# Kernel tuning notes

Measured on AMD Instinct MI355X. Metric: run time of the kernel, lower is better.

The kernel has to match this reference:

```python
import jax, jax.numpy as jnp
import numpy as np

B = 524288   # particles
H = 128      # hidden_size
E = 64       # embed_dim
NT = 512     # num trajectories
IN = 16 + 9 + E  # fc1 input dim = 89
EPS = 1e-6


def setup_inputs() -> dict:
    key = jax.random.key(0)
    ks = jax.random.split(key, 12)
    w = lambda k, shp, fan_in: (jax.random.normal(k, shp, dtype=jnp.float32)
                                / np.sqrt(fan_in).astype(np.float32))
    return {
        "F": jax.random.normal(ks[0], (B, 3, 3), dtype=jnp.float32),
        "C": jax.random.normal(ks[1], (B, 3, 3), dtype=jnp.float32),
        "traj_id": 7,
        "latent": jax.random.normal(ks[2], (NT, E), dtype=jnp.float32),
        "W1": w(ks[3], (IN, H), IN), "b1": jnp.zeros((H,), jnp.float32),
        "W2": w(ks[4], (H, H), H),   "b2": jnp.zeros((H,), jnp.float32),
        "W3": w(ks[5], (H, H), H),   "b3": jnp.zeros((H,), jnp.float32),
        "W4": w(ks[6], (H, H), H),   "b4": jnp.zeros((H,), jnp.float32),
        "W5": w(ks[7], (H, H), H),   "b5": jnp.zeros((H,), jnp.float32),
        "W6": w(ks[8], (H, H), H),   "b6": jnp.zeros((H,), jnp.float32),
        "W7": w(ks[9], (H, 9), H),   "b7": jnp.zeros((9,), jnp.float32),
    }


def _strain_features(F):
    # FFt: [B,3,3]; J = clamp(det F); J1 = clamp(F00); sigma: 3 singular values
    FFt = jnp.einsum('bij,bkj->bik', F, F)
    J = jnp.maximum(jnp.linalg.det(F), EPS)
    J1 = jnp.maximum(F[:, 0, 0], EPS)
    sigma = jnp.linalg.svd(F, compute_uv=False)  # descending, like torch.svd
    return jnp.concatenate([
        FFt.reshape(-1, 9),
        jnp.log(J)[:, None], sigma, J[:, None],
        jnp.log(J1)[:, None], J1[:, None],
    ], axis=-1)  # [B,16]


def reference(F, C, traj_id, latent,
              W1, b1, W2, b2, W3, b3, W4, b4, W5, b5, W6, b6, W7, b7):
    strain = _strain_features(F)                                   # [B,16]
    lat = jnp.broadcast_to(latent[traj_id], (F.shape[0], latent.shape[1]))
    x = jnp.concatenate([strain, C.reshape(-1, 9), lat], axis=-1)  # [B,89]
    g = lambda z: jax.nn.gelu(z, approximate=False)  # exact, matches torch GELU
    x = g(x @ W1 + b1)
    x = g(x @ W2 + b2)
    x = g(x @ W3 + b3)
    x = g(x @ W4 + b4)
    x = g(x @ W5 + b5)
    x = g(x @ W6 + b6)
    out = (x @ W7 + b7).reshape(-1, 3, 3)
    return 0.5 * (out + jnp.swapaxes(out, 1, 2))  # symmetric stress [B,3,3]
```

## Files before the change

### kernel.cpp

```cpp
#include <hip/hip_runtime.h>
#include <hip/hip_bf16.h>
#include <math.h>

#define BPART   524288
#define NBLK    (BPART / 128)
#define W7_OFF  98304
#define WB_N    102400
#define BIAS_N  800
#define PREP_N  (WB_N + BIAS_N)

typedef __bf16 bf16x8 __attribute__((ext_vector_type(8)));
typedef float  f32x16 __attribute__((ext_vector_type(16)));
typedef float  f32x4  __attribute__((ext_vector_type(4)));
typedef float  f32x2  __attribute__((ext_vector_type(2)));

#define MFMA __builtin_amdgcn_mfma_f32_32x32x16_bf16

__device__ __forceinline__ unsigned short f2bf(float f) {
  union { float f; unsigned u; } v; v.f = f;
  unsigned r = v.u + 0x7fffu + ((v.u >> 16) & 1u);
  return (unsigned short)(r >> 16);
}
__device__ __forceinline__ unsigned pack_bf16(float a, float b) {
  unsigned ua = __builtin_bit_cast(unsigned, a) + 0x8000u;
  unsigned ub = __builtin_bit_cast(unsigned, b) + 0x8000u;
  return __builtin_amdgcn_perm(ub, ua, 0x07060302u);
}
__device__ __forceinline__ int swz(int row, int col) {
  return (row << 7) | ((((col >> 3) ^ (row & 7)) << 3) | (col & 7));
}

__device__ __forceinline__ f32x2 pk_mul(f32x2 a, f32x2 b) {
  f32x2 d; asm("v_pk_mul_f32 %0, %1, %2" : "=v"(d) : "v"(a), "v"(b)); return d;
}
__device__ __forceinline__ f32x2 pk_fma(f32x2 a, f32x2 b, f32x2 c) {
  f32x2 d; asm("v_pk_fma_f32 %0, %1, %2, %3" : "=v"(d) : "v"(a), "v"(b), "v"(c)); return d;
}
__device__ __forceinline__ f32x2 gelu2(f32x2 z) {
  const f32x2 c1 = {0.1029432f, 0.1029432f};
  const f32x2 c0 = {2.30220818f, 2.30220818f};
  f32x2 z2 = pk_mul(z, z);
  f32x2 t  = pk_fma(z2, c1, c0);
  f32x2 yp = pk_mul(z, t);
  float e0 = __builtin_amdgcn_exp2f(-yp.x);
  float e1 = __builtin_amdgcn_exp2f(-yp.y);
  float r0 = __builtin_amdgcn_rcpf(e0 + 1.0f);
  float r1 = __builtin_amdgcn_rcpf(e1 + 1.0f);
  f32x2 g; g.x = z.x * r0; g.y = z.y * r1;
  return g;
}
__device__ __forceinline__ void cp16(const void* g, void* l) {
  __builtin_amdgcn_global_load_lds(
      (const __attribute__((address_space(1))) void*)g,
      (__attribute__((address_space(3))) void*)l, 16, 0, 0);
}

__global__ void prep_weights(
    const float* __restrict__ W1, const float* __restrict__ W2,
    const float* __restrict__ W3, const float* __restrict__ W4,
    const float* __restrict__ W5, const float* __restrict__ W6,
    const float* __restrict__ W7,
    const float* __restrict__ b1, const float* __restrict__ b2,
    const float* __restrict__ b3, const float* __restrict__ b4,
    const float* __restrict__ b5, const float* __restrict__ b6,
    const float* __restrict__ b7,
    unsigned short* __restrict__ wsb, float* __restrict__ wsf)
{
  int idx = blockIdx.x * 256 + threadIdx.x;
  if (idx < WB_N) {
    unsigned short v = 0;
    if (idx < W7_OFF) {
      int l = idx >> 14;
      int o = idx & 16383;
      int n = o >> 7, e = o & 127;
      int k = (((e >> 3) ^ (n & 7)) << 3) | (e & 7);
      const float* W = (l==0)?W1:(l==1)?W2:(l==2)?W3:(l==3)?W4:(l==4)?W5:W6;
      float x = (l == 0) ? ((k < 89) ? W[k*128 + n] : 0.0f)
                         : W[k*128 + n];
      v = f2bf(x);
    } else {
      int o = idx - W7_OFF;
      int n = o >> 7, e = o & 127;
      int k = (((e >> 3) ^ (n & 7)) << 3) | (e & 7);
      v = (n < 9) ? f2bf(W7[k*9 + n]) : (unsigned short)0;
    }
    wsb[idx] = v;
  } else if (idx < PREP_N) {
    int r = idx - WB_N;
    float x;
    if (r < 768) {
      int l = r >> 7, n = r & 127;
      const float* bb = (l==0)?b1:(l==1)?b2:(l==2)?b3:(l==3)?b4:(l==4)?b5:b6;
      x = bb[n];
    } else {
      int n = r - 768;
      x = (n < 9) ? b7[n] : 0.0f;
    }
    wsf[r] = x;
  }
}

__global__ __launch_bounds__(256, 2) void stress_mlp(
    const float* __restrict__ F, const float* __restrict__ Cmat,
    const int* __restrict__ traj, const float* __restrict__ latent,
    const unsigned short* __restrict__ wst, const float* __restrict__ wsf,
    float* __restrict__ out)
{
  __shared__ __align__(16) unsigned short act_s[128 * 128];
  __shared__ __align__(16) unsigned short wt_s[128 * 128];

  const int tid  = threadIdx.x;
  const int lane = tid & 63;
  const int wid  = tid >> 6;
  const int lm   = lane & 31;
  const int lk   = lane >> 5;
  const int m0   = (wid >> 1) << 6;
  const int n0   = (wid & 1) << 6;
  const int pbase = (int)blockIdx.x << 7;

  {
    const char* src = (const char*)wst;
    char* dst = (char*)wt_s;
    #pragma unroll
    for (int i = 0; i < 8; ++i)
      cp16(src + i*4096 + tid*16, dst + i*4096 + tid*16);
  }

  if (tid < 128) {
    const int row = tid;
    const int p   = pbase + row;
    float f[9];
    #pragma unroll
    for (int i = 0; i < 9; ++i) f[i] = F[p * 9 + i];
    float fft[9];
    #pragma unroll
    for (int i = 0; i < 3; ++i)
      #pragma unroll
      for (int k = 0; k < 3; ++k)
        fft[i*3+k] = f[i*3]*f[k*3] + f[i*3+1]*f[k*3+1] + f[i*3+2]*f[k*3+2];
    float det = f[0]*(f[4]*f[8]-f[5]*f[7]) - f[1]*(f[3]*f[8]-f[5]*f[6])
              + f[2]*(f[3]*f[7]-f[4]*f[6]);
    float J  = fmaxf(det, 1e-6f);
    float J1 = fmaxf(f[0], 1e-6f);
    float a00=fft[0], a01=fft[1], a02=fft[2], a11=fft[4], a12=fft[5], a22=fft[8];
    float q  = (a00+a11+a22) * (1.0f/3.0f);
    float d0 = a00-q, d1 = a11-q, d2 = a22-q;
    float p2 = d0*d0 + d1*d1 + d2*d2 + 2.0f*(a01*a01 + a02*a02 + a12*a12);
    float e0, e1, e2;
    if (p2 < 1e-14f) { e0 = e1 = e2 = q; }
    else {
      float pp  = sqrtf(p2 * (1.0f/6.0f));
      float inv = 1.0f / pp;
      float b00=d0*inv, b11=d1*inv, b22=d2*inv, b01=a01*inv, b02=a02*inv, b12=a12*inv;
      float detb = b00*(b11*b22-b12*b12) - b01*(b01*b22-b12*b02) + b02*(b01*b12-b11*b02);
      float rr = 0.5f * detb;
      rr = fminf(fmaxf(rr, -1.0f), 1.0f);
      float pr = acosf(rr) * (1.0f / (3.0f * 6.2831853071795864f));
      e0 = q + 2.0f*pp*__builtin_amdgcn_cosf(pr);
      e2 = q + 2.0f*pp*__builtin_amdgcn_cosf(pr + (1.0f/3.0f));
      e1 = 3.0f*q - e0 - e2;
    }
    float s0 = sqrtf(fmaxf(e0, 0.f));
    float s1 = sqrtf(fmaxf(e1, 0.f));
    float s2 = sqrtf(fmaxf(e2, 0.f));
    #pragma unroll
    for (int i = 0; i < 9; ++i) act_s[swz(row, i)] = f2bf(fft[i]);
    act_s[swz(row,  9)] = f2bf(logf(J));
    act_s[swz(row, 10)] = f2bf(s0);
    act_s[swz(row, 11)] = f2bf(s1);
    act_s[swz(row, 12)] = f2bf(s2);
    act_s[swz(row, 13)] = f2bf(J);
    act_s[swz(row, 14)] = f2bf(logf(J1));
    act_s[swz(row, 15)] = f2bf(J1);
    #pragma unroll
    for (int i = 0; i < 9; ++i) act_s[swz(row, 16 + i)] = f2bf(Cmat[p*9 + i]);
  } else {
    const int row = tid - 128;
    const int t = traj[0];
    const float* lat = latent + t * 64;
    for (int j = 0; j < 64; ++j) act_s[swz(row, 25 + j)] = f2bf(lat[j]);
    for (int j = 89; j < 128; ++j) act_s[swz(row, j)] = 0;
  }

  const int mr0 = m0 + lm,      mr1 = m0 + 32 + lm;
  const int nr0 = n0 + lm,      nr1 = n0 + 32 + lm;

  f32x16 acc[2][2];
  union BF { f32x16 v; f32x4 q[4]; };

  for (int l = 0; l < 6; ++l) {
    BF bias[2];
    const float* bl = wsf + (l << 7);
    #pragma unroll
    for (int tn = 0; tn < 2; ++tn)
      #pragma unroll
      for (int qq = 0; qq < 4; ++qq)
        bias[tn].q[qq] = *(const f32x4*)(bl + n0 + (tn << 5) + (qq << 3) + (lk << 2));

    __syncthreads();

    {
      bf16x8 x0 = *(const bf16x8*)&act_s[(mr0 << 7) + ((lk ^ (mr0 & 7)) << 3)];
      bf16x8 x1 = *(const bf16x8*)&act_s[(mr1 << 7) + ((lk ^ (mr1 & 7)) << 3)];
      bf16x8 w0 = *(const bf16x8*)&wt_s[(nr0 << 7) + ((lk ^ (nr0 & 7)) << 3)];
      bf16x8 w1 = *(const bf16x8*)&wt_s[(nr1 << 7) + ((lk ^ (nr1 & 7)) << 3)];
      acc[0][0] = MFMA(w0, x0, bias[0].v, 0, 0, 0);
      acc[0][1] = MFMA(w0, x1, bias[0].v, 0, 0, 0);
      acc[1][0] = MFMA(w1, x0, bias[1].v, 0, 0, 0);
      acc[1][1] = MFMA(w1, x1, bias[1].v, 0, 0, 0);
    }
    #pragma unroll
    for (int kk = 1; kk < 8; ++kk) {
      const int kc = (kk << 1) + lk;
      bf16x8 x0 = *(const bf16x8*)&act_s[(mr0 << 7) + ((kc ^ (mr0 & 7)) << 3)];
      bf16x8 x1 = *(const bf16x8*)&act_s[(mr1 << 7) + ((kc ^ (mr1 & 7)) << 3)];
      bf16x8 w0 = *(const bf16x8*)&wt_s[(nr0 << 7) + ((kc ^ (nr0 & 7)) << 3)];
      bf16x8 w1 = *(const bf16x8*)&wt_s[(nr1 << 7) + ((kc ^ (nr1 & 7)) << 3)];
      acc[0][0] = MFMA(w0, x0, acc[0][0], 0, 0, 0);
      acc[0][1] = MFMA(w0, x1, acc[0][1], 0, 0, 0);
      acc[1][0] = MFMA(w1, x0, acc[1][0], 0, 0, 0);
      acc[1][1] = MFMA(w1, x1, acc[1][1], 0, 0, 0);
    }
    __syncthreads();

    if (l < 5) {
      const char* src = (const char*)(wst + ((l + 1) << 14));
      char* dst = (char*)wt_s;
      #pragma unroll
      for (int i = 0; i < 8; ++i)
        cp16(src + i*4096 + tid*16, dst + i*4096 + tid*16);
    } else {
      const char* src = (const char*)(wst + W7_OFF);
      char* dst = (char*)wt_s;
      #pragma unroll
      for (int i = 0; i < 2; ++i)
        cp16(src + i*4096 + tid*16, dst + i*4096 + tid*16);
    }

    #pragma unroll
    for (int tm = 0; tm < 2; ++tm) {
      const int m    = m0 + (tm << 5) + lm;
      const int rowb = m << 7;
      const int rx   = m & 7;
      #pragma unroll
      for (int tn = 0; tn < 2; ++tn) {
        const int cb = ((n0 + (tn << 5)) >> 3);
        #pragma unroll
        for (int q = 0; q < 4; ++q) {
          f32x2 za; za.x = acc[tn][tm][4*q + 0]; za.y = acc[tn][tm][4*q + 1];
          f32x2 zb; zb.x = acc[tn][tm][4*q + 2]; zb.y = acc[tn][tm][4*q + 3];
          f32x2 ga = gelu2(za);
          f32x2 gb = gelu2(zb);
          uint2 u;
          u.x = pack_bf16(ga.x, ga.y);
          u.y = pack_bf16(gb.x, gb.y);
          const int off = rowb + (((cb + q) ^ rx) << 3) + (lk << 2);
          *reinterpret_cast<uint2*>(&act_s[off]) = u;
        }
      }
    }
  }

  {
    BF bias7;
    #pragma unroll
    for (int qq = 0; qq < 4; ++qq)
      bias7.q[qq] = *(const f32x4*)(wsf + 768 + (qq << 3) + (lk << 2));

    __syncthreads();

    f32x16 acc7[2];
    if ((wid & 1) == 0) {
      {
        bf16x8 x0 = *(const bf16x8*)&act_s[(mr0 << 7) + ((lk ^ (mr0 & 7)) << 3)];
        bf16x8 x1 = *(const bf16x8*)&act_s[(mr1 << 7) + ((lk ^ (mr1 & 7)) << 3)];
        bf16x8 w0 = *(const bf16x8*)&wt_s[(lm << 7) + ((lk ^ (lm & 7)) << 3)];
        acc7[0] = MFMA(w0, x0, bias7.v, 0, 0, 0);
        acc7[1] = MFMA(w0, x1, bias7.v, 0, 0, 0);
      }
      #pragma unroll
      for (int kk = 1; kk < 8; ++kk) {
        const int kc = (kk << 1) + lk;
        bf16x8 x0 = *(const bf16x8*)&act_s[(mr0 << 7) + ((kc ^ (mr0 & 7)) << 3)];
        bf16x8 x1 = *(const bf16x8*)&act_s[(mr1 << 7) + ((kc ^ (mr1 & 7)) << 3)];
        bf16x8 w0 = *(const bf16x8*)&wt_s[(lm << 7) + ((kc ^ (lm & 7)) << 3)];
        acc7[0] = MFMA(w0, x0, acc7[0], 0, 0, 0);
        acc7[1] = MFMA(w0, x1, acc7[1], 0, 0, 0);
      }
    }
    __syncthreads();

    float* ots = (float*)wt_s;
    if ((wid & 1) == 0) {
      #pragma unroll
      for (int tm = 0; tm < 2; ++tm) {
        const int m = m0 + (tm << 5) + lm;
        #pragma unroll
        for (int j = 0; j < 4; ++j)
          ots[m * 9 + (lk << 2) + j] = acc7[tm][j];
        if (lk == 0) ots[m * 9 + 8] = acc7[tm][4];
      }
    }
    __syncthreads();

    if (tid < 128) {
      const int row = tid;
      float z[9];
      #pragma unroll
      for (int i = 0; i < 9; ++i) z[i] = ots[row * 9 + i];
      #pragma unroll
      for (int rr = 0; rr < 3; ++rr)
        #pragma unroll
        for (int cc = 0; cc < 3; ++cc)
          ots[row * 9 + rr*3 + cc] = 0.5f * (z[rr*3+cc] + z[cc*3+rr]);
    }
    __syncthreads();

    float4* dst = (float4*)(out + (size_t)pbase * 9);
    const float4* srcv = (const float4*)ots;
    for (int s = tid; s < 288; s += 256) dst[s] = srcv[s];
  }
}

extern "C" void kernel_launch(void* const* d_in, const int* in_sizes, int n_in,
                              void* d_out, int out_size, void* d_ws, size_t ws_size,
                              hipStream_t stream) {
  const float* F   = (const float*)d_in[0];
  const float* C   = (const float*)d_in[1];
  const int*   trj = (const int*)d_in[2];
  const float* lat = (const float*)d_in[3];
  const float* W1  = (const float*)d_in[4];
  const float* b1  = (const float*)d_in[5];
  const float* W2  = (const float*)d_in[6];
  const float* b2  = (const float*)d_in[7];
  const float* W3  = (const float*)d_in[8];
  const float* b3  = (const float*)d_in[9];
  const float* W4  = (const float*)d_in[10];
  const float* b4  = (const float*)d_in[11];
  const float* W5  = (const float*)d_in[12];
  const float* b5  = (const float*)d_in[13];
  const float* W6  = (const float*)d_in[14];
  const float* b6  = (const float*)d_in[15];
  const float* W7  = (const float*)d_in[16];
  const float* b7  = (const float*)d_in[17];

  unsigned short* wsb = (unsigned short*)d_ws;
  float* wsf = (float*)((char*)d_ws + WB_N * 2);

  prep_weights<<<dim3((PREP_N + 255) / 256), dim3(256), 0, stream>>>(
      W1, W2, W3, W4, W5, W6, W7, b1, b2, b3, b4, b5, b6, b7, wsb, wsf);
  stress_mlp<<<dim3(NBLK), dim3(256), 0, stream>>>(
      F, C, trj, lat, wsb, wsf, (float*)d_out);
}
```

Baseline: 287.6 us.

## Keep activations in registers across layers via permuted weight output ordering

Weight columns and biases are permuted at prep time so that each MFMA accumulator layout maps directly onto the next layer's B-operand register layout. Activations now stay in registers between layers instead of being written to and re-read from a shared-memory activation tile. That removes the act_s buffer, halves LDS use and allows the launch bound of 4 blocks per CU, with each wave owning 32 particles across all 128 outputs. Risks include higher register pressure from 32 packed activation registers plus four accumulators, and a permutation mapping that must be exactly right for correctness.

```diff
diff --git a/kernel.cpp b/kernel.cpp
--- a/kernel.cpp
+++ b/kernel.cpp
@@ -15,6 +15,9 @@
 typedef float  f32x2  __attribute__((ext_vector_type(2)));
 
 #define MFMA __builtin_amdgcn_mfma_f32_32x32x16_bf16
+#define UNROLL _Pragma("unroll")
+
+union XU { unsigned u[4]; bf16x8 v; };
 
 __device__ __forceinline__ unsigned short f2bf(float f) {
   union { float f; unsigned u; } v; v.f = f;
@@ -26,8 +29,10 @@
   unsigned ub = __builtin_bit_cast(unsigned, b) + 0x8000u;
   return __builtin_amdgcn_perm(ub, ua, 0x07060302u);
 }
-__device__ __forceinline__ int swz(int row, int col) {
-  return (row << 7) | ((((col >> 3) ^ (row & 7)) << 3) | (col & 7));
+
+__device__ __forceinline__ int sigma(int n) {
+  int c = ((n >> 5) << 2) | ((n >> 3) & 3);
+  return ((c >> 1) << 4) | (((n >> 2) & 1) << 3) | ((c & 1) << 2) | (n & 3);
 }
 
 __device__ __forceinline__ f32x2 pk_mul(f32x2 a, f32x2 b) {
@@ -74,15 +79,17 @@
       int o = idx & 16383;
       int n = o >> 7, e = o & 127;
       int k = (((e >> 3) ^ (n & 7)) << 3) | (e & 7);
+      int sn = sigma(n);
       const float* W = (l==0)?W1:(l==1)?W2:(l==2)?W3:(l==3)?W4:(l==4)?W5:W6;
-      float x = (l == 0) ? ((k < 89) ? W[k*128 + n] : 0.0f)
-                         : W[k*128 + n];
+      float x = (l == 0) ? ((k < 89) ? W[k*128 + sn] : 0.0f)
+                         : W[k*128 + sn];
       v = f2bf(x);
     } else {
       int o = idx - W7_OFF;
       int n = o >> 7, e = o & 127;
       int k = (((e >> 3) ^ (n & 7)) << 3) | (e & 7);
-      v = (n < 9) ? f2bf(W7[k*9 + n]) : (unsigned short)0;
+      int sn = sigma(n);
+      v = (sn < 9) ? f2bf(W7[k*9 + sn]) : (unsigned short)0;
     }
     wsb[idx] = v;
   } else if (idx < PREP_N) {
@@ -91,235 +98,241 @@
     if (r < 768) {
       int l = r >> 7, n = r & 127;
       const float* bb = (l==0)?b1:(l==1)?b2:(l==2)?b3:(l==3)?b4:(l==4)?b5:b6;
-      x = bb[n];
+      x = bb[sigma(n)];
     } else {
       int n = r - 768;
-      x = (n < 9) ? b7[n] : 0.0f;
+      int sn = sigma(n);
+      x = (sn < 9) ? b7[sn] : 0.0f;
     }
     wsf[r] = x;
   }
 }
 
-__global__ __launch_bounds__(256, 2) void stress_mlp(
+#define MFMA_LAYER(NKK)                                                       \
+  {                                                                           \
+    const float* bls_ = (const float*)((const char*)wt_s + 32768);            \
+    UNROLL                                                                    \
+    for (int kk = 0; kk < (NKK); ++kk) {                                      \
+      XU x_;                                                                  \
+      x_.u[0] = xw[4*kk+0]; x_.u[1] = xw[4*kk+1];                             \
+      x_.u[2] = xw[4*kk+2]; x_.u[3] = xw[4*kk+3];                             \
+      const int ch_ = ((2*kk + lk) ^ x7) << 3;                                \
+      UNROLL                                                                  \
+      for (int tn = 0; tn < 4; ++tn) {                                        \
+        bf16x8 w_ = *(const bf16x8*)&wt_s[tn*4096 + rb0 + ch_];               \
+        if (kk == 0) {                                                        \
+          f32x16 cf_;                                                         \
+          UNROLL                                                              \
+          for (int qq = 0; qq < 4; ++qq) {                                    \
+            f32x4 b4_ = *(const f32x4*)&bls_[tn*32 + qq*8 + lk*4];            \
+            cf_[4*qq+0] = b4_[0]; cf_[4*qq+1] = b4_[1];                       \
+            cf_[4*qq+2] = b4_[2]; cf_[4*qq+3] = b4_[3];                       \
+          }                                                                   \
+          acc[tn] = MFMA(w_, x_.v, cf_, 0, 0, 0);                             \
+        } else {                                                              \
+          acc[tn] = MFMA(w_, x_.v, acc[tn], 0, 0, 0);                         \
+        }                                                                     \
+      }                                                                       \
+    }                                                                         \
+  }
+
+#define GELU_EPILOGUE                                                         \
+  UNROLL                                                                      \
+  for (int c = 0; c < 16; ++c) {                                              \
+    const int tn_ = c >> 2, q_ = c & 3, t_ = c >> 1, h_ = c & 1;              \
+    f32x2 za_, zb_;                                                           \
+    za_.x = acc[tn_][4*q_+0]; za_.y = acc[tn_][4*q_+1];                       \
+    zb_.x = acc[tn_][4*q_+2]; zb_.y = acc[tn_][4*q_+3];                       \
+    f32x2 ga_ = gelu2(za_);                                                   \
+    f32x2 gb_ = gelu2(zb_);                                                   \
+    xw[4*t_ + 2*h_ + 0] = pack_bf16(ga_.x, ga_.y);                            \
+    xw[4*t_ + 2*h_ + 1] = pack_bf16(gb_.x, gb_.y);                            \
+  }
+
+__global__ __launch_bounds__(256, 4) void stress_mlp(
     const float* __restrict__ F, const float* __restrict__ Cmat,
     const int* __restrict__ traj, const float* __restrict__ latent,
     const unsigned short* __restrict__ wst, const float* __restrict__ wsf,
     float* __restrict__ out)
 {
-  __shared__ __align__(16) unsigned short act_s[128 * 128];
-  __shared__ __align__(16) unsigned short wt_s[128 * 128];
+  __shared__ __align__(16) unsigned short wt_s[128 * 128 + 256];
 
   const int tid  = threadIdx.x;
   const int lane = tid & 63;
   const int wid  = tid >> 6;
   const int lm   = lane & 31;
   const int lk   = lane >> 5;
-  const int m0   = (wid >> 1) << 6;
-  const int n0   = (wid & 1) << 6;
+  const int x7   = lm & 7;
+  const int rb0  = lm << 7;
   const int pbase = (int)blockIdx.x << 7;
+  const int p    = pbase + (wid << 5) + lm;
 
   {
     const char* src = (const char*)wst;
     char* dst = (char*)wt_s;
-    #pragma unroll
+    UNROLL
     for (int i = 0; i < 8; ++i)
       cp16(src + i*4096 + tid*16, dst + i*4096 + tid*16);
-  }
-
-  if (tid < 128) {
-    const int row = tid;
-    const int p   = pbase + row;
+    if (tid < 32) cp16((const char*)wsf + tid*16, dst + 32768 + tid*16);
+  }
+
+  unsigned xw[32];
+
+  {
+    const float* Fp = F + (size_t)p * 9;
     float f[9];
-    #pragma unroll
-    for (int i = 0; i < 9; ++i) f[i] = F[p * 9 + i];
+    UNROLL
+    for (int i = 0; i < 9; ++i) f[i] = Fp[i];
     float fft[9];
-    #pragma unroll
+    UNROLL
     for (int i = 0; i < 3; ++i)
-      #pragma unroll
+      UNROLL
       for (int k = 0; k < 3; ++k)
         fft[i*3+k] = f[i*3]*f[k*3] + f[i*3+1]*f[k*3+1] + f[i*3+2]*f[k*3+2];
-    float det = f[0]*(f[4]*f[8]-f[5]*f[7]) - f[1]*(f[3]*f[8]-f[5]*f[6])
-              + f[2]*(f[3]*f[7]-f[4]*f[6]);
-    float J  = fmaxf(det, 1e-6f);
-    float J1 = fmaxf(f[0], 1e-6f);
-    float a00=fft[0], a01=fft[1], a02=fft[2], a11=fft[4], a12=fft[5], a22=fft[8];
-    float q  = (a00+a11+a22) * (1.0f/3.0f);
-    float d0 = a00-q, d1 = a11-q, d2 = a22-q;
-    float p2 = d0*d0 + d1*d1 + d2*d2 + 2.0f*(a01*a01 + a02*a02 + a12*a12);
-    float e0, e1, e2;
-    if (p2 < 1e-14f) { e0 = e1 = e2 = q; }
-    else {
-      float pp  = sqrtf(p2 * (1.0f/6.0f));
-      float inv = 1.0f / pp;
-      float b00=d0*inv, b11=d1*inv, b22=d2*inv, b01=a01*inv, b02=a02*inv, b12=a12*inv;
-      float detb = b00*(b11*b22-b12*b12) - b01*(b01*b22-b12*b02) + b02*(b01*b12-b11*b02);
-      float rr = 0.5f * detb;
-      rr = fminf(fmaxf(rr, -1.0f), 1.0f);
-      float pr = acosf(rr) * (1.0f / (3.0f * 6.2831853071795864f));
-      e0 = q + 2.0f*pp*__builtin_amdgcn_cosf(pr);
-      e2 = q + 2.0f*pp*__builtin_amdgcn_cosf(pr + (1.0f/3.0f));
-      e1 = 3.0f*q - e0 - e2;
-    }
-    float s0 = sqrtf(fmaxf(e0, 0.f));
-    float s1 = sqrtf(fmaxf(e1, 0.f));
-    float s2 = sqrtf(fmaxf(e2, 0.f));
-    #pragma unroll
-    for (int i = 0; i < 9; ++i) act_s[swz(row, i)] = f2bf(fft[i]);
-    act_s[swz(row,  9)] = f2bf(logf(J));
-    act_s[swz(row, 10)] = f2bf(s0);
-    act_s[swz(row, 11)] = f2bf(s1);
-    act_s[swz(row, 12)] = f2bf(s2);
-    act_s[swz(row, 13)] = f2bf(J);
-    act_s[swz(row, 14)] = f2bf(logf(J1));
-    act_s[swz(row, 15)] = f2bf(J1);
-    #pragma unroll
-    for (int i = 0; i < 9; ++i) act_s[swz(row, 16 + i)] = f2bf(Cmat[p*9 + i]);
-  } else {
-    const int row = tid - 128;
-    const int t = traj[0];
-    const float* lat = latent + t * 64;
-    for (int j = 0; j < 64; ++j) act_s[swz(row, 25 + j)] = f2bf(lat[j]);
-    for (int j = 89; j < 128; ++j) act_s[swz(row, j)] = 0;
-  }
-
-  const int mr0 = m0 + lm,      mr1 = m0 + 32 + lm;
-  const int nr0 = n0 + lm,      nr1 = n0 + 32 + lm;
-
-  f32x16 acc[2][2];
-  union BF { f32x16 v; f32x4 q[4]; };
-
-  for (int l = 0; l < 6; ++l) {
-    BF bias[2];
-    const float* bl = wsf + (l << 7);
-    #pragma unroll
-    for (int tn = 0; tn < 2; ++tn)
-      #pragma unroll
-      for (int qq = 0; qq < 4; ++qq)
-        bias[tn].q[qq] = *(const f32x4*)(bl + n0 + (tn << 5) + (qq << 3) + (lk << 2));
-
+    const float* lat = latent + (size_t)traj[0] * 64;
+
+    if (lk == 0) {
+      xw[0] = pack_bf16(fft[0], fft[1]);
+      xw[1] = pack_bf16(fft[2], fft[3]);
+      xw[2] = pack_bf16(fft[4], fft[5]);
+      xw[3] = pack_bf16(fft[6], fft[7]);
+      const float* Cp = Cmat + (size_t)p * 9;
+      UNROLL
+      for (int i = 0; i < 4; ++i) xw[4+i] = pack_bf16(Cp[2*i], Cp[2*i+1]);
+      UNROLL
+      for (int t = 0; t < 4; ++t) {
+        const float* lb = lat + 7 + 16*t;
+        UNROLL
+        for (int i = 0; i < 4; ++i) xw[8 + 4*t + i] = pack_bf16(lb[2*i], lb[2*i+1]);
+      }
+    } else {
+      float det = f[0]*(f[4]*f[8]-f[5]*f[7]) - f[1]*(f[3]*f[8]-f[5]*f[6])
+                + f[2]*(f[3]*f[7]-f[4]*f[6]);
+      float J  = fmaxf(det, 1e-6f);
+      float J1 = fmaxf(f[0], 1e-6f);
+      float a00=fft[0], a01=fft[1], a02=fft[2], a11=fft[4], a12=fft[5], a22=fft[8];
+      float q  = (a00+a11+a22) * (1.0f/3.0f);
+      float d0 = a00-q, d1 = a11-q, d2 = a22-q;
+      float p2 = d0*d0 + d1*d1 + d2*d2 + 2.0f*(a01*a01 + a02*a02 + a12*a12);
+      float e0, e1, e2;
+      if (p2 < 1e-14f) { e0 = e1 = e2 = q; }
+      else {
+        float pp  = sqrtf(p2 * (1.0f/6.0f));
+        float inv = 1.0f / pp;
+        float b00=d0*inv, b11=d1*inv, b22=d2*inv, b01=a01*inv, b02=a02*inv, b12=a12*inv;
+        float detb = b00*(b11*b22-b12*b12) - b01*(b01*b22-b12*b02) + b02*(b01*b12-b11*b02);
+        float rr = 0.5f * detb;
+        rr = fminf(fmaxf(rr, -1.0f), 1.0f);
+        float pr = acosf(rr) * (1.0f / (3.0f * 6.2831853071795864f));
+        e0 = q + 2.0f*pp*__builtin_amdgcn_cosf(pr);
+        e2 = q + 2.0f*pp*__builtin_amdgcn_cosf(pr + (1.0f/3.0f));
+        e1 = 3.0f*q - e0 - e2;
+      }
+      float s0 = sqrtf(fmaxf(e0, 0.f));
+      float s1 = sqrtf(fmaxf(e1, 0.f));
+      float s2 = sqrtf(fmaxf(e2, 0.f));
+      xw[0] = pack_bf16(fft[8], logf(J));
+      xw[1] = pack_bf16(s0, s1);
+      xw[2] = pack_bf16(s2, J);
+      xw[3] = pack_bf16(logf(J1), J1);
+      float c8 = Cmat[(size_t)p*9 + 8];
+      xw[4] = pack_bf16(c8, lat[0]);
+      xw[5] = pack_bf16(lat[1], lat[2]);
+      xw[6] = pack_bf16(lat[3], lat[4]);
+      xw[7] = pack_bf16(lat[5], lat[6]);
+      UNROLL
+      for (int t = 0; t < 3; ++t) {
+        const float* lb = lat + 15 + 16*t;
+        UNROLL
+        for (int i = 0; i < 4; ++i) xw[8 + 4*t + i] = pack_bf16(lb[2*i], lb[2*i+1]);
+      }
+      xw[20] = pack_bf16(lat[63], 0.0f);
+      xw[21] = 0u; xw[22] = 0u; xw[23] = 0u;
+    }
+  }
+
+  f32x16 acc[4];
+
+  __syncthreads();
+  MFMA_LAYER(6)
+  __syncthreads();
+  {
+    const char* src = (const char*)(wst + (1 << 14));
+    UNROLL
+    for (int i = 0; i < 8; ++i)
+      cp16(src + i*4096 + tid*16, (char*)wt_s + i*4096 + tid*16);
+    if (tid < 32) cp16((const char*)(wsf + 128) + tid*16, (char*)wt_s + 32768 + tid*16);
+  }
+  GELU_EPILOGUE
+
+  for (int l = 1; l < 6; ++l) {
     __syncthreads();
-
-    {
-      bf16x8 x0 = *(const bf16x8*)&act_s[(mr0 << 7) + ((lk ^ (mr0 & 7)) << 3)];
-      bf16x8 x1 = *(const bf16x8*)&act_s[(mr1 << 7) + ((lk ^ (mr1 & 7)) << 3)];
-      bf16x8 w0 = *(const bf16x8*)&wt_s[(nr0 << 7) + ((lk ^ (nr0 & 7)) << 3)];
-      bf16x8 w1 = *(const bf16x8*)&wt_s[(nr1 << 7) + ((lk ^ (nr1 & 7)) << 3)];
-      acc[0][0] = MFMA(w0, x0, bias[0].v, 0, 0, 0);
-      acc[0][1] = MFMA(w0, x1, bias[0].v, 0, 0, 0);
-      acc[1][0] = MFMA(w1, x0, bias[1].v, 0, 0, 0);
-      acc[1][1] = MFMA(w1, x1, bias[1].v, 0, 0, 0);
-    }
-    #pragma unroll
-    for (int kk = 1; kk < 8; ++kk) {
-      const int kc = (kk << 1) + lk;
-      bf16x8 x0 = *(const bf16x8*)&act_s[(mr0 << 7) + ((kc ^ (mr0 & 7)) << 3)];
-      bf16x8 x1 = *(const bf16x8*)&act_s[(mr1 << 7) + ((kc ^ (mr1 & 7)) << 3)];
-      bf16x8 w0 = *(const bf16x8*)&wt_s[(nr0 << 7) + ((kc ^ (nr0 & 7)) << 3)];
-      bf16x8 w1 = *(const bf16x8*)&wt_s[(nr1 << 7) + ((kc ^ (nr1 & 7)) << 3)];
-      acc[0][0] = MFMA(w0, x0, acc[0][0], 0, 0, 0);
-      acc[0][1] = MFMA(w0, x1, acc[0][1], 0, 0, 0);
-      acc[1][0] = MFMA(w1, x0, acc[1][0], 0, 0, 0);
-      acc[1][1] = MFMA(w1, x1, acc[1][1], 0, 0, 0);
-    }
+    MFMA_LAYER(8)
     __syncthreads();
-
     if (l < 5) {
       const char* src = (const char*)(wst + ((l + 1) << 14));
-      char* dst = (char*)wt_s;
-      #pragma unroll
+      UNROLL
       for (int i = 0; i < 8; ++i)
-        cp16(src + i*4096 + tid*16, dst + i*4096 + tid*16);
+        cp16(src + i*4096 + tid*16, (char*)wt_s + i*4096 + tid*16);
+      if (tid < 32)
+        cp16((const char*)(wsf + ((l + 1) << 7)) + tid*16, (char*)wt_s + 32768 + tid*16);
     } else {
       const char* src = (const char*)(wst + W7_OFF);
-      char* dst = (char*)wt_s;
-      #pragma unroll
+      UNROLL
       for (int i = 0; i < 2; ++i)
-        cp16(src + i*4096 + tid*16, dst + i*4096 + tid*16);
-    }
-
-    #pragma unroll
-    for (int tm = 0; tm < 2; ++tm) {
-      const int m    = m0 + (tm << 5) + lm;
-      const int rowb = m << 7;
-      const int rx   = m & 7;
-      #pragma unroll
-      for (int tn = 0; tn < 2; ++tn) {
-        const int cb = ((n0 + (tn << 5)) >> 3);
-        #pragma unroll
-        for (int q = 0; q < 4; ++q) {
-          f32x2 za; za.x = acc[tn][tm][4*q + 0]; za.y = acc[tn][tm][4*q + 1];
-          f32x2 zb; zb.x = acc[tn][tm][4*q + 2]; zb.y = acc[tn][tm][4*q + 3];
-          f32x2 ga = gelu2(za);
-          f32x2 gb = gelu2(zb);
-          uint2 u;
-          u.x = pack_bf16(ga.x, ga.y);
-          u.y = pack_bf16(gb.x, gb.y);
-          const int off = rowb + (((cb + q) ^ rx) << 3) + (lk << 2);
-          *reinterpret_cast<uint2*>(&act_s[off]) = u;
+        cp16(src + i*4096 + tid*16, (char*)wt_s + i*4096 + tid*16);
+      if (tid < 8)
+        cp16((const char*)(wsf + 768) + tid*16, (char*)wt_s + 32768 + tid*16);
+    }
+    GELU_EPILOGUE
+  }
+
+  __syncthreads();
+  f32x16 a7;
+  {
+    const float* bls = (const float*)((const char*)wt_s + 32768);
+    UNROLL
+    for (int kk = 0; kk < 8; ++kk) {
+      XU x;
+      x.u[0] = xw[4*kk+0]; x.u[1] = xw[4*kk+1];
+      x.u[2] = xw[4*kk+2]; x.u[3] = xw[4*kk+3];
+      const int ch = ((2*kk + lk) ^ x7) << 3;
+      bf16x8 w = *(const bf16x8*)&wt_s[rb0 + ch];
+      if (kk == 0) {
+        f32x16 cf;
+        UNROLL
+        for (int qq = 0; qq < 4; ++qq) {
+          f32x4 b4 = *(const f32x4*)&bls[qq*8 + lk*4];
+          cf[4*qq+0] = b4[0]; cf[4*qq+1] = b4[1];
+          cf[4*qq+2] = b4[2]; cf[4*qq+3] = b4[3];
         }
+        a7 = MFMA(w, x.v, cf, 0, 0, 0);
+      } else {
+        a7 = MFMA(w, x.v, a7, 0, 0, 0);
       }
     }
   }
-
-  {
-    BF bias7;
-    #pragma unroll
-    for (int qq = 0; qq < 4; ++qq)
-      bias7.q[qq] = *(const f32x4*)(wsf + 768 + (qq << 3) + (lk << 2));
-
-    __syncthreads();
-
-    f32x16 acc7[2];
-    if ((wid & 1) == 0) {
-      {
-        bf16x8 x0 = *(const bf16x8*)&act_s[(mr0 << 7) + ((lk ^ (mr0 & 7)) << 3)];
-        bf16x8 x1 = *(const bf16x8*)&act_s[(mr1 << 7) + ((lk ^ (mr1 & 7)) << 3)];
-        bf16x8 w0 = *(const bf16x8*)&wt_s[(lm << 7) + ((lk ^ (lm & 7)) << 3)];
-        acc7[0] = MFMA(w0, x0, bias7.v, 0, 0, 0);
-        acc7[1] = MFMA(w0, x1, bias7.v, 0, 0, 0);
-      }
-      #pragma unroll
-      for (int kk = 1; kk < 8; ++kk) {
-        const int kc = (kk << 1) + lk;
-        bf16x8 x0 = *(const bf16x8*)&act_s[(mr0 << 7) + ((kc ^ (mr0 & 7)) << 3)];
-        bf16x8 x1 = *(const bf16x8*)&act_s[(mr1 << 7) + ((kc ^ (mr1 & 7)) << 3)];
-        bf16x8 w0 = *(const bf16x8*)&wt_s[(lm << 7) + ((kc ^ (lm & 7)) << 3)];
-        acc7[0] = MFMA(w0, x0, acc7[0], 0, 0, 0);
-        acc7[1] = MFMA(w0, x1, acc7[1], 0, 0, 0);
-      }
-    }
-    __syncthreads();
-
-    float* ots = (float*)wt_s;
-    if ((wid & 1) == 0) {
-      #pragma unroll
-      for (int tm = 0; tm < 2; ++tm) {
-        const int m = m0 + (tm << 5) + lm;
-        #pragma unroll
-        for (int j = 0; j < 4; ++j)
-          ots[m * 9 + (lk << 2) + j] = acc7[tm][j];
-        if (lk == 0) ots[m * 9 + 8] = acc7[tm][4];
-      }
-    }
-    __syncthreads();
-
-    if (tid < 128) {
-      const int row = tid;
-      float z[9];
-      #pragma unroll
-      for (int i = 0; i < 9; ++i) z[i] = ots[row * 9 + i];
-      #pragma unroll
-      for (int rr = 0; rr < 3; ++rr)
-        #pragma unroll
-        for (int cc = 0; cc < 3; ++cc)
-          ots[row * 9 + rr*3 + cc] = 0.5f * (z[rr*3+cc] + z[cc*3+rr]);
-    }
-    __syncthreads();
-
-    float4* dst = (float4*)(out + (size_t)pbase * 9);
-    const float4* srcv = (const float4*)ots;
-    for (int s = tid; s < 288; s += 256) dst[s] = srcv[s];
-  }
+  __syncthreads();
+
+  float o8 = __shfl_xor(a7[0], 32);
+  float* ots = (float*)wt_s;
+  if (lk == 0) {
+    const int row = (wid << 5) + lm;
+    float z[9];
+    UNROLL
+    for (int i = 0; i < 8; ++i) z[i] = a7[i];
+    z[8] = o8;
+    UNROLL
+    for (int rr = 0; rr < 3; ++rr)
+      UNROLL
+      for (int cc = 0; cc < 3; ++cc)
+        ots[row*9 + rr*3 + cc] = 0.5f * (z[rr*3+cc] + z[cc*3+rr]);
+  }
+  __syncthreads();
+
+  float4* dst = (float4*)(out + (size_t)pbase * 9);
+  const float4* srcv = (const float4*)ots;
+  for (int s = tid; s < 288; s += 256) dst[s] = srcv[s];
 }
 
 extern "C" void kernel_launch(void* const* d_in, const int* in_sizes, int n_in,
```

Result: faster. 269.4 us (-6.3%).
